# Performance work log

Hardware: AMD Instinct MI355X
Metric: run time of the kernel (lower is better)

The kernel has to match this reference:

```python
import jax, jax.numpy as jnp
import numpy as np

B, L, P, A = 32, 512, 128, 128   # batch, prot seq len, prot dim, atom dim
N = 1024                          # total atoms (32 per molecule)
H1, H2 = 512, 256                 # hidden_list


def setup_inputs() -> dict:
    key = jax.random.key(0)
    ks = jax.random.split(key, 12)
    atom_embed = jax.random.normal(ks[0], (N, A), dtype=jnp.float32)
    protSeq_embed = jax.random.normal(ks[1], (B, L, P), dtype=jnp.float32)
    # sorted segment ids, every segment non-empty (32 atoms per molecule)
    atom_splits = jnp.repeat(jnp.arange(B, dtype=jnp.int64), N // B)
    s = 0.05
    att1_W = jax.random.normal(ks[2], (P + A, 128), dtype=jnp.float32) * s
    att1_b = jnp.zeros((128,), dtype=jnp.float32)
    att2_W = jax.random.normal(ks[3], (128, 1), dtype=jnp.float32) * s
    att2_b = jnp.zeros((1,), dtype=jnp.float32)
    d1_W = jax.random.normal(ks[4], (A + P, H1), dtype=jnp.float32) * s
    d1_b = jnp.zeros((H1,), dtype=jnp.float32)
    d2_W = jax.random.normal(ks[5], (H1, H2), dtype=jnp.float32) * s
    d2_b = jnp.zeros((H2,), dtype=jnp.float32)
    out_W = jax.random.normal(ks[6], (H2, 1), dtype=jnp.float32) * s
    out_b = jnp.zeros((1,), dtype=jnp.float32)
    return {"atom_embed": atom_embed, "protSeq_embed": protSeq_embed,
            "atom_splits": atom_splits,
            "att1_W": att1_W, "att1_b": att1_b, "att2_W": att2_W, "att2_b": att2_b,
            "d1_W": d1_W, "d1_b": d1_b, "d2_W": d2_W, "d2_b": d2_b,
            "out_W": out_W, "out_b": out_b}


def reference(atom_embed, protSeq_embed, atom_splits,
              att1_W, att1_b, att2_W, att2_b,
              d1_W, d1_b, d2_W, d2_b, out_W, out_b):
    num_seg = protSeq_embed.shape[0]
    # gather protein rows per atom: [N, L, P]
    prot_g = protSeq_embed[atom_splits]
    # concat with broadcast atom embed: [N, L, P+A]
    atom_x = jnp.broadcast_to(atom_embed[:, None, :], prot_g.shape[:2] + atom_embed.shape[-1:])
    concat = jnp.concatenate([prot_g, atom_x], axis=-1)
    # attention MLP -> scores W: [N, L]
    hid = jnp.tanh(concat @ att1_W + att1_b)
    W = 5.0 * jnp.tanh(hid @ att2_W + att2_b)[..., 0]
    # atom-side weights: exp(max over seq), normalized per segment
    Wc = jnp.exp(jnp.max(W, axis=-1, keepdims=True))                     # [N, 1]
    Sc = jax.ops.segment_sum(Wc, atom_splits, num_segments=num_seg)[atom_splits]
    aa = Wc / Sc                                                          # [N, 1]
    atom_pool = jax.ops.segment_sum(aa * atom_embed, atom_splits, num_segments=num_seg)  # [B, A]
    # protein-side: segment-max scores, softmax over seq, weighted sum
    Wp = jax.ops.segment_max(W, atom_splits, num_segments=num_seg)       # [B, L]
    ap = jax.nn.softmax(Wp, axis=-1)
    prot_pool = jnp.einsum('bl,bld->bd', ap, protSeq_embed)              # [B, P]
    z = jnp.concatenate([atom_pool, prot_pool], axis=-1)
    z = jax.nn.relu(z @ d1_W + d1_b)
    z = jax.nn.relu(z @ d2_W + d2_b)
    return z @ out_W + out_b                                             # [B, 1]
```

## Files before the change

### kernel.cpp

```cpp
#include <hip/hip_runtime.h>
#include <math.h>

#define BSEG 32
#define LSEQ 512

__device__ __forceinline__ float fast_tanh(float x) {
    x = fminf(fmaxf(x, -20.0f), 20.0f);
    float e = __expf(2.0f * x);
    return __fdividef(e - 1.0f, e + 1.0f);
}
__device__ __forceinline__ float trm(float c, float p, float e) {
    return c * __builtin_amdgcn_rcpf(fmaf(p, e, 1.0f));
}
__device__ __forceinline__ float clexp2(float v) {
    return __expf(2.0f * fminf(fmaxf(v, -20.0f), 20.0f));
}

__device__ __forceinline__ void gemm32_exp(
    const float* __restrict__ Xrow0, const float* __restrict__ Wm,
    const float* __restrict__ bias, float* __restrict__ xs,
    float* __restrict__ ws, float* __restrict__ dst, int dstride, int tid)
{
    #pragma unroll
    for (int t = 0; t < 4; ++t) {
        int flat = (tid + 256 * t) * 4;
        int r = flat >> 7, k4 = flat & 127;
        *(float4*)&xs[r * 132 + k4] = *(const float4*)&Xrow0[r * 128 + k4];
    }
    const int tx = tid & 31, ty = tid >> 5;
    float acc[4][4];
    #pragma unroll
    for (int i = 0; i < 4; ++i)
        #pragma unroll
        for (int j = 0; j < 4; ++j) acc[i][j] = 0.0f;
    #pragma unroll
    for (int q = 0; q < 4; ++q) {
        #pragma unroll
        for (int t = 0; t < 4; ++t) {
            int flat = (tid + 256 * t) * 4;
            int kk = flat >> 7, c4 = flat & 127;
            *(float4*)&ws[kk * 132 + c4] =
                *(const float4*)&Wm[(q * 32 + kk) * 128 + c4];
        }
        __syncthreads();
        #pragma unroll 2
        for (int kg = 0; kg < 8; ++kg) {
            float4 A[4];
            #pragma unroll
            for (int r = 0; r < 4; ++r)
                A[r] = *(const float4*)&xs[(4 * ty + r) * 132 + q * 32 + kg * 4];
            #pragma unroll
            for (int j = 0; j < 4; ++j) {
                float4 b4 = *(const float4*)&ws[(kg * 4 + j) * 132 + 4 * tx];
                #pragma unroll
                for (int r = 0; r < 4; ++r) {
                    float av = ((const float*)&A[r])[j];
                    acc[r][0] += av * b4.x; acc[r][1] += av * b4.y;
                    acc[r][2] += av * b4.z; acc[r][3] += av * b4.w;
                }
            }
        }
        __syncthreads();
    }
    float b4v[4] = {0.f, 0.f, 0.f, 0.f};
    if (bias) *(float4*)b4v = *(const float4*)&bias[4 * tx];
    #pragma unroll
    for (int i = 0; i < 4; ++i) {
        float4 o;
        o.x = clexp2(acc[i][0] + b4v[0]);
        o.y = clexp2(acc[i][1] + b4v[1]);
        o.z = clexp2(acc[i][2] + b4v[2]);
        o.w = clexp2(acc[i][3] + b4v[3]);
        *(float4*)&dst[(4 * ty + i) * dstride + 4 * tx] = o;
    }
}

__global__ __launch_bounds__(256) void eb_kernel(
    const float* __restrict__ atom_embed, const float* __restrict__ Wa,
    float* __restrict__ eb)
{
    __shared__ float smem[8448];
    const int b = blockIdx.x;
    gemm32_exp(atom_embed + (long)b * 32 * 128, Wa, nullptr,
               smem, smem + 4224, eb + (long)b * 32 * 128, 128, threadIdx.x);
}

__global__ __launch_bounds__(256, 2) void fused_kernel(
    const float* __restrict__ eb, const float* __restrict__ protSeq,
    const float* __restrict__ att1_W, const float* __restrict__ att1_b,
    const float* __restrict__ att2_W, const float* __restrict__ att2_b,
    const float* __restrict__ out_b,
    float* __restrict__ pmax, float* __restrict__ zrp,
    float* __restrict__ dpp, float* __restrict__ out)
{
    __shared__ float smem[16896];
    float* eps = smem;
    float* ebs = smem + 4224;
    float* xs  = smem + 8448;
    float* ws  = smem + 12672;
    float* c_s  = smem + 8448;
    float* pmn  = smem + 8576;
    float* wps  = smem + 9664;
    float* es   = smem + 9696;
    float* part = smem + 9728;
    float* scal = smem + 9984;

    const int tid = threadIdx.x;
    const int chunk = blockIdx.x, b = blockIdx.y;
    const int lbase = chunk * 32;

    if (chunk == 0 && tid == 0) out[b] = out_b[0];

    #pragma unroll
    for (int t = 0; t < 4; ++t) {
        int flat = (tid + 256 * t) * 4;
        int n = flat >> 7, j = flat & 127;
        *(float4*)&ebs[n * 132 + j] = *(const float4*)&eb[(b * 32 + n) * 128 + j];
    }

    gemm32_exp(protSeq + ((long)(b * 512 + lbase)) * 128, att1_W, att1_b,
               xs, ws, eps, 132, tid);

    if (tid < 128) c_s[tid] = -2.0f * att2_W[tid];
    __syncthreads();
    if (tid < 64) {
        float s = c_s[tid] + c_s[tid + 64];
        #pragma unroll
        for (int m = 1; m < 64; m <<= 1) s += __shfl_xor(s, m);
        if (tid == 0) scal[0] = -0.5f * s + att2_b[0];
    }
    __syncthreads();

    const int ng = tid & 7, lg = tid >> 3;
    const float* qp  = &eps[lg * 132];
    const float* b0p = &ebs[ng * 132];
    const float* b1p = &ebs[(ng + 8) * 132];
    const float* b2p = &ebs[(ng + 16) * 132];
    const float* b3p = &ebs[(ng + 24) * 132];
    float a0 = 0.f, a1 = 0.f, a2 = 0.f, a3 = 0.f;
    #pragma unroll 4
    for (int jj = 0; jj < 128; jj += 4) {
        float4 c4 = *(const float4*)&c_s[jj];
        float4 q  = *(const float4*)(qp + jj);
        float4 b0 = *(const float4*)(b0p + jj);
        float4 b1 = *(const float4*)(b1p + jj);
        float4 b2 = *(const float4*)(b2p + jj);
        float4 b3 = *(const float4*)(b3p + jj);
        a0 += trm(c4.x, q.x, b0.x); a1 += trm(c4.x, q.x, b1.x);
        a2 += trm(c4.x, q.x, b2.x); a3 += trm(c4.x, q.x, b3.x);
        a0 += trm(c4.y, q.y, b0.y); a1 += trm(c4.y, q.y, b1.y);
        a2 += trm(c4.y, q.y, b2.y); a3 += trm(c4.y, q.y, b3.y);
        a0 += trm(c4.z, q.z, b0.z); a1 += trm(c4.z, q.z, b1.z);
        a2 += trm(c4.z, q.z, b2.z); a3 += trm(c4.z, q.z, b3.z);
        a0 += trm(c4.w, q.w, b0.w); a1 += trm(c4.w, q.w, b1.w);
        a2 += trm(c4.w, q.w, b2.w); a3 += trm(c4.w, q.w, b3.w);
    }
    const float bs = scal[0];
    float W0 = 5.0f * fast_tanh(a0 + bs);
    float W1 = 5.0f * fast_tanh(a1 + bs);
    float W2 = 5.0f * fast_tanh(a2 + bs);
    float W3 = 5.0f * fast_tanh(a3 + bs);

    float m = fmaxf(fmaxf(W0, W1), fmaxf(W2, W3));
    #pragma unroll
    for (int d = 1; d < 8; d <<= 1) m = fmaxf(m, __shfl_xor(m, d));
    if (ng == 0) wps[lg] = m;
    pmn[lg * 34 + ng]      = W0;
    pmn[lg * 34 + ng + 8]  = W1;
    pmn[lg * 34 + ng + 16] = W2;
    pmn[lg * 34 + ng + 24] = W3;
    __syncthreads();
    if (tid < 32) {
        float mm = pmn[tid];
        #pragma unroll
        for (int g = 1; g < 32; ++g) mm = fmaxf(mm, pmn[g * 34 + tid]);
        pmax[b * 512 + chunk * 32 + tid] = mm;
        es[tid] = __expf(wps[tid]);
    }
    __syncthreads();
    if (tid < 32) {
        float v = es[tid];
        #pragma unroll
        for (int d = 1; d < 32; d <<= 1) v += __shfl_xor(v, d);
        if (tid == 0) dpp[b * 16 + chunk] = v;
    }
    const int dd = tid & 127, hf = tid >> 7;
    float az = 0.0f;
    #pragma unroll 4
    for (int i = 0; i < 16; ++i)
        az += es[hf * 16 + i] *
              protSeq[((long)(b * 512 + lbase + hf * 16 + i)) * 128 + dd];
    part[tid] = az;
    __syncthreads();
    if (tid < 128) zrp[(b * 16 + chunk) * 128 + tid] = part[tid] + part[128 + tid];
}

__global__ __launch_bounds__(256) void mlp1_kernel(
    const float* __restrict__ pmax, const float* __restrict__ zrp,
    const float* __restrict__ dpp, const float* __restrict__ atom_embed,
    const float* __restrict__ d1_W, const float* __restrict__ d1_b,
    float* __restrict__ h1)
{
    __shared__ float zs[256];
    __shared__ float part[4 * 65];
    __shared__ float expw[32];
    __shared__ float sc[2];
    const int tid = threadIdx.x;
    const int cx = blockIdx.x, b = blockIdx.y;

    if (tid < 32) {
        float m = -1e30f;
        #pragma unroll
        for (int c = 0; c < 16; ++c) m = fmaxf(m, pmax[b * 512 + c * 32 + tid]);
        float e = __expf(m);
        expw[tid] = e;
        #pragma unroll
        for (int d = 1; d < 32; d <<= 1) e += __shfl_xor(e, d);
        if (tid == 0) sc[0] = 1.0f / e;
    }
    if (tid == 64) {
        float s = 0.0f;
        #pragma unroll
        for (int c = 0; c < 16; ++c) s += dpp[b * 16 + c];
        sc[1] = 1.0f / s;
    }
    __syncthreads();
    if (tid < 128) {
        float a = 0.0f;
        #pragma unroll 8
        for (int n = 0; n < 32; ++n)
            a += expw[n] * atom_embed[(b * 32 + n) * 128 + tid];
        zs[tid] = a * sc[0];
    } else {
        int d = tid - 128;
        float a = 0.0f;
        #pragma unroll
        for (int c = 0; c < 16; ++c) a += zrp[(b * 16 + c) * 128 + d];
        zs[tid] = a * sc[1];
    }
    __syncthreads();
    const int c0 = cx * 64, ci = tid & 63, kg = tid >> 6;
    float acc = 0.0f;
    #pragma unroll 8
    for (int k = kg * 64; k < kg * 64 + 64; ++k)
        acc += zs[k] * d1_W[k * 512 + c0 + ci];
    part[kg * 65 + ci] = acc;
    __syncthreads();
    if (tid < 64) {
        float s = part[tid] + part[65 + tid] + part[130 + tid] + part[195 + tid]
                + d1_b[c0 + tid];
        h1[b * 512 + c0 + tid] = fmaxf(s, 0.0f);
    }
}

__global__ __launch_bounds__(256) void mlp2_kernel(
    const float* __restrict__ h1, const float* __restrict__ d2_W,
    const float* __restrict__ d2_b, const float* __restrict__ out_W,
    float* __restrict__ out)
{
    __shared__ float hs[512];
    __shared__ float part[8 * 33];
    const int tid = threadIdx.x;
    const int c0 = blockIdx.x * 32, b = blockIdx.y;
    hs[tid] = h1[b * 512 + tid];
    hs[tid + 256] = h1[b * 512 + 256 + tid];
    __syncthreads();
    const int ci = tid & 31, kg = tid >> 5;
    float acc = 0.0f;
    #pragma unroll 8
    for (int k = kg * 64; k < kg * 64 + 64; ++k)
        acc += hs[k] * d2_W[k * 256 + c0 + ci];
    part[kg * 33 + ci] = acc;
    __syncthreads();
    if (tid < 32) {
        float s = d2_b[c0 + tid];
        #pragma unroll
        for (int g = 0; g < 8; ++g) s += part[g * 33 + tid];
        float contrib = fmaxf(s, 0.0f) * out_W[c0 + tid];
        #pragma unroll
        for (int d = 1; d < 32; d <<= 1) contrib += __shfl_xor(contrib, d);
        if (tid == 0) atomicAdd(&out[b], contrib);
    }
}

extern "C" void kernel_launch(void* const* d_in, const int* in_sizes, int n_in,
                              void* d_out, int out_size, void* d_ws, size_t ws_size,
                              hipStream_t stream) {
    const float* atom_embed = (const float*)d_in[0];
    const float* protSeq    = (const float*)d_in[1];
    const float* att1_W = (const float*)d_in[3];
    const float* att1_b = (const float*)d_in[4];
    const float* att2_W = (const float*)d_in[5];
    const float* att2_b = (const float*)d_in[6];
    const float* d1_W   = (const float*)d_in[7];
    const float* d1_b   = (const float*)d_in[8];
    const float* d2_W   = (const float*)d_in[9];
    const float* d2_b   = (const float*)d_in[10];
    const float* out_W  = (const float*)d_in[11];
    const float* out_b  = (const float*)d_in[12];
    float* out = (float*)d_out;

    float* ws = (float*)d_ws;
    float* eb   = ws;
    float* pmax = eb + 131072;
    float* zrp  = pmax + 16384;
    float* dpp  = zrp + 65536;
    float* h1   = dpp + 512;

    eb_kernel<<<BSEG, 256, 0, stream>>>(atom_embed, att1_W + 128 * 128, eb);
    fused_kernel<<<dim3(16, BSEG), 256, 0, stream>>>(
        eb, protSeq, att1_W, att1_b, att2_W, att2_b, out_b,
        pmax, zrp, dpp, out);
    mlp1_kernel<<<dim3(8, BSEG), 256, 0, stream>>>(
        pmax, zrp, dpp, atom_embed, d1_W, d1_b, h1);
    mlp2_kernel<<<dim3(8, BSEG), 256, 0, stream>>>(
        h1, d2_W, d2_b, out_W, out);
}
```

Before: 123.9 us.

## Fuse atom-side exp GEMM into main kernel, prefetch MLP weights, widen MLP grids

Removes the separate eb_kernel: each fused block now recomputes the atom-side exp(atom@Wa) GEMM for its molecule straight into shared memory, trading redundant compute (16x per molecule) for one fewer launch and no global round-trip. Each block also reads a stripe of d1_W/d2_W into a dummy sum to warm L2 for the later MLP kernels, guarded by a never-true store. The prot-pool weighted sum now reads the protein tile still held in shared memory (xs) instead of global. The MLP kernels use twice as many blocks with smaller column tiles for more parallelism.

```diff
diff --git a/kernel.cpp b/kernel.cpp
--- a/kernel.cpp
+++ b/kernel.cpp
@@ -75,35 +75,27 @@
     }
 }
 
-__global__ __launch_bounds__(256) void eb_kernel(
-    const float* __restrict__ atom_embed, const float* __restrict__ Wa,
-    float* __restrict__ eb)
-{
-    __shared__ float smem[8448];
-    const int b = blockIdx.x;
-    gemm32_exp(atom_embed + (long)b * 32 * 128, Wa, nullptr,
-               smem, smem + 4224, eb + (long)b * 32 * 128, 128, threadIdx.x);
-}
-
 __global__ __launch_bounds__(256, 2) void fused_kernel(
-    const float* __restrict__ eb, const float* __restrict__ protSeq,
+    const float* __restrict__ atom_embed, const float* __restrict__ protSeq,
     const float* __restrict__ att1_W, const float* __restrict__ att1_b,
     const float* __restrict__ att2_W, const float* __restrict__ att2_b,
+    const float* __restrict__ d1_W, const float* __restrict__ d2_W,
     const float* __restrict__ out_b,
     float* __restrict__ pmax, float* __restrict__ zrp,
-    float* __restrict__ dpp, float* __restrict__ out)
+    float* __restrict__ dpp, float* __restrict__ out,
+    float* __restrict__ dummy)
 {
     __shared__ float smem[16896];
     float* eps = smem;
     float* ebs = smem + 4224;
     float* xs  = smem + 8448;
     float* ws  = smem + 12672;
-    float* c_s  = smem + 8448;
-    float* pmn  = smem + 8576;
-    float* wps  = smem + 9664;
-    float* es   = smem + 9696;
-    float* part = smem + 9728;
-    float* scal = smem + 9984;
+    float* c_s  = smem + 12672;
+    float* pmn  = smem + 12800;
+    float* wps  = smem + 13888;
+    float* es   = smem + 13920;
+    float* part = smem + 13952;
+    float* scal = smem + 14208;
 
     const int tid = threadIdx.x;
     const int chunk = blockIdx.x, b = blockIdx.y;
@@ -111,13 +103,21 @@
 
     if (chunk == 0 && tid == 0) out[b] = out_b[0];
 
-    #pragma unroll
-    for (int t = 0; t < 4; ++t) {
-        int flat = (tid + 256 * t) * 4;
-        int n = flat >> 7, j = flat & 127;
-        *(float4*)&ebs[n * 132 + j] = *(const float4*)&eb[(b * 32 + n) * 128 + j];
-    }
-
+    float wsum = 0.0f;
+    {
+        const int fb = chunk + 16 * b;
+        const int stripe = ((fb >> 3) + ((fb & 7) << 3)) & 63;
+        #pragma unroll
+        for (int t = 0; t < 4; ++t) {
+            int idx = stripe * 1024 + t * 256 + tid;
+            const float* base = (idx < 32768) ? d1_W : d2_W;
+            float4 v = *(const float4*)&base[(idx & 32767) * 4];
+            wsum += v.x + v.y + v.z + v.w;
+        }
+    }
+
+    gemm32_exp(atom_embed + (long)b * 32 * 128, att1_W + 128 * 128, nullptr,
+               xs, ws, ebs, 132, tid);
     gemm32_exp(protSeq + ((long)(b * 512 + lbase)) * 128, att1_W, att1_b,
                xs, ws, eps, 132, tid);
 
@@ -188,11 +188,12 @@
     float az = 0.0f;
     #pragma unroll 4
     for (int i = 0; i < 16; ++i)
-        az += es[hf * 16 + i] *
-              protSeq[((long)(b * 512 + lbase + hf * 16 + i)) * 128 + dd];
+        az += es[hf * 16 + i] * xs[(hf * 16 + i) * 132 + dd];
     part[tid] = az;
     __syncthreads();
     if (tid < 128) zrp[(b * 16 + chunk) * 128 + tid] = part[tid] + part[128 + tid];
+
+    if (wsum == 1.0e38f) dummy[0] = wsum;
 }
 
 __global__ __launch_bounds__(256) void mlp1_kernel(
@@ -202,7 +203,7 @@
     float* __restrict__ h1)
 {
     __shared__ float zs[256];
-    __shared__ float part[4 * 65];
+    __shared__ float part[8 * 33];
     __shared__ float expw[32];
     __shared__ float sc[2];
     const int tid = threadIdx.x;
@@ -239,16 +240,17 @@
         zs[tid] = a * sc[1];
     }
     __syncthreads();
-    const int c0 = cx * 64, ci = tid & 63, kg = tid >> 6;
+    const int c0 = cx * 32, ci = tid & 31, kg = tid >> 5;
     float acc = 0.0f;
     #pragma unroll 8
-    for (int k = kg * 64; k < kg * 64 + 64; ++k)
+    for (int k = kg * 32; k < kg * 32 + 32; ++k)
         acc += zs[k] * d1_W[k * 512 + c0 + ci];
-    part[kg * 65 + ci] = acc;
-    __syncthreads();
-    if (tid < 64) {
-        float s = part[tid] + part[65 + tid] + part[130 + tid] + part[195 + tid]
-                + d1_b[c0 + tid];
+    part[kg * 33 + ci] = acc;
+    __syncthreads();
+    if (tid < 32) {
+        float s = d1_b[c0 + tid];
+        #pragma unroll
+        for (int g = 0; g < 8; ++g) s += part[g * 33 + tid];
         h1[b * 512 + c0 + tid] = fmaxf(s, 0.0f);
     }
 }
@@ -259,26 +261,26 @@
     float* __restrict__ out)
 {
     __shared__ float hs[512];
-    __shared__ float part[8 * 33];
+    __shared__ float part[16 * 17];
     const int tid = threadIdx.x;
-    const int c0 = blockIdx.x * 32, b = blockIdx.y;
+    const int c0 = blockIdx.x * 16, b = blockIdx.y;
     hs[tid] = h1[b * 512 + tid];
     hs[tid + 256] = h1[b * 512 + 256 + tid];
     __syncthreads();
-    const int ci = tid & 31, kg = tid >> 5;
+    const int ci = tid & 15, kg = tid >> 4;
     float acc = 0.0f;
     #pragma unroll 8
-    for (int k = kg * 64; k < kg * 64 + 64; ++k)
+    for (int k = kg * 32; k < kg * 32 + 32; ++k)
         acc += hs[k] * d2_W[k * 256 + c0 + ci];
-    part[kg * 33 + ci] = acc;
-    __syncthreads();
-    if (tid < 32) {
+    part[kg * 17 + ci] = acc;
+    __syncthreads();
+    if (tid < 16) {
         float s = d2_b[c0 + tid];
         #pragma unroll
-        for (int g = 0; g < 8; ++g) s += part[g * 33 + tid];
+        for (int g = 0; g < 16; ++g) s += part[g * 17 + tid];
         float contrib = fmaxf(s, 0.0f) * out_W[c0 + tid];
         #pragma unroll
-        for (int d = 1; d < 32; d <<= 1) contrib += __shfl_xor(contrib, d);
+        for (int d = 1; d < 16; d <<= 1) contrib += __shfl_xor(contrib, d);
         if (tid == 0) atomicAdd(&out[b], contrib);
     }
 }
@@ -301,18 +303,17 @@
     float* out = (float*)d_out;
 
     float* ws = (float*)d_ws;
-    float* eb   = ws;
-    float* pmax = eb + 131072;
-    float* zrp  = pmax + 16384;
-    float* dpp  = zrp + 65536;
-    float* h1   = dpp + 512;
-
-    eb_kernel<<<BSEG, 256, 0, stream>>>(atom_embed, att1_W + 128 * 128, eb);
+    float* pmax  = ws;
+    float* zrp   = pmax + 16384;
+    float* dpp   = zrp + 65536;
+    float* h1    = dpp + 512;
+    float* dummy = h1 + 16384;
+
     fused_kernel<<<dim3(16, BSEG), 256, 0, stream>>>(
-        eb, protSeq, att1_W, att1_b, att2_W, att2_b, out_b,
-        pmax, zrp, dpp, out);
-    mlp1_kernel<<<dim3(8, BSEG), 256, 0, stream>>>(
+        atom_embed, protSeq, att1_W, att1_b, att2_W, att2_b,
+        d1_W, d2_W, out_b, pmax, zrp, dpp, out, dummy);
+    mlp1_kernel<<<dim3(16, BSEG), 256, 0, stream>>>(
         pmax, zrp, dpp, atom_embed, d1_W, d1_b, h1);
-    mlp2_kernel<<<dim3(8, BSEG), 256, 0, stream>>>(
+    mlp2_kernel<<<dim3(16, BSEG), 256, 0, stream>>>(
         h1, d2_W, d2_b, out_W, out);
 }
```

After: 121.3 us. 2.1% less time.
